# Kernel tuning notes

Measured on AMD Instinct MI355X. Metric: run time of the kernel, lower is better.

## Reference

```python
import jax, jax.numpy as jnp
import numpy as np

N, D = 8192, 128
TEMPERATURE = 0.07
EPS = 1e-8
NEG_FILL = -9e15


def setup_inputs() -> dict:
    key = jax.random.key(0)
    feats = jax.random.normal(key, (N, D), dtype=jnp.float32)
    # SimCLR-style positive-pair mask: row i's positive is row (i + N//2) % N.
    # Exactly one positive per row, as required by the original broadcast.
    label = jnp.roll(jnp.eye(N, dtype=jnp.int32), N // 2, axis=1)
    return {"feats": feats, "label": label}


def reference(feats, label):
    # F.cosine_similarity clamps each norm at eps before dividing.
    norms = jnp.linalg.norm(feats, axis=-1, keepdims=True)
    nf = feats / jnp.maximum(norms, EPS)            # [N, D] unit rows
    cos_sim = nf @ nf.T                             # [N, N] cosine similarities
    n = cos_sim.shape[0]
    self_mask = jnp.eye(n, dtype=bool)
    cos_sim = jnp.where(self_mask, NEG_FILL, cos_sim)
    cos_sim = cos_sim / TEMPERATURE
    pos_mask = (label == 1)
    # Exactly one positive per row -> masked sum == cos_sim[pos_mask] in row order.
    pos = jnp.sum(jnp.where(pos_mask, cos_sim, 0.0), axis=-1)  # [N]
    lse = jax.nn.logsumexp(cos_sim, axis=-1)                    # [N]
    return jnp.mean(-pos + lse)
```

## Files before the change

### kernel.cpp

```cpp
#include <hip/hip_runtime.h>


#define NN 8192
#define DD 128

typedef __bf16 bf16x8 __attribute__((ext_vector_type(8)));
typedef float f32x4 __attribute__((ext_vector_type(4)));
typedef unsigned int u32x4 __attribute__((ext_vector_type(4)));

constexpr float kM     = 1.0f / 0.07f;
constexpr float kScale = 1.4426950408889634f / 0.07f;
constexpr float kLn2   = 0.6931471805599453f;

__device__ inline unsigned short f2bf(float f) {
  unsigned int u = __float_as_uint(f);
  unsigned int r = (u + 0x7FFFu + ((u >> 16) & 1u)) >> 16;
  return (unsigned short)r;
}

__global__ __launch_bounds__(256) void k_normalize(const float* __restrict__ feats,
                                                   unsigned short* __restrict__ nfb) {
  int tid = threadIdx.x;
  int lane = tid & 63;
  int row = blockIdx.x * 4 + (tid >> 6);
  float2 f = *(const float2*)(feats + (size_t)row * DD + lane * 2);
  float ss = f.x * f.x + f.y * f.y;
  #pragma unroll
  for (int m = 1; m < 64; m <<= 1) ss += __shfl_xor(ss, m);
  float rn = 1.0f / fmaxf(sqrtf(ss), 1e-8f);
  unsigned int lo = f2bf(f.x * rn), hi = f2bf(f.y * rn);
  *(unsigned int*)(nfb + (size_t)row * DD + lane * 2) = lo | (hi << 16);
}

__global__ __launch_bounds__(256) void k_fused(const unsigned short* __restrict__ nfb,
                                               const int* __restrict__ label,
                                               float* __restrict__ lpart,
                                               int* __restrict__ pos_idx) {
  __shared__ __align__(16) unsigned short ldsB[64 * DD];
  int g = blockIdx.x;
  int tid = threadIdx.x;
  int r0 = (g >> 2) * 64;
  int c0 = (g & 3) * 2048;
  int lane = tid & 63, w = tid >> 6;
  int wm = w >> 1, wn = w & 1;
  int lg = lane >> 4;
  int ll = lane & 15;

  const u32x4* L = (const u32x4*)label;
  int sbase = g * 32768 + tid;

  bf16x8 afr[2][4];
  #pragma unroll
  for (int ms = 0; ms < 2; ms++) {
    const unsigned short* arow = nfb + (size_t)(r0 + wm * 32 + ms * 16 + ll) * DD + lg * 8;
    #pragma unroll
    for (int kc = 0; kc < 4; kc++)
      afr[ms][kc] = *(const bf16x8*)(arow + kc * 32);
  }

  float lacc[2][4] = {{0.f, 0.f, 0.f, 0.f}, {0.f, 0.f, 0.f, 0.f}};
  int slr = tid >> 4;
  int sch = tid & 15;

  for (int ct = 0; ct < 32; ct++) {
    int ctile = c0 + ct * 64;
    __syncthreads();
    #pragma unroll
    for (int p = 0; p < 4; p++) {
      int row = p * 16 + slr;
      u32x4 v = *(const u32x4*)(nfb + (size_t)(ctile + row) * DD + sch * 8);
      *(u32x4*)((char*)ldsB + row * 256 + ((sch * 16) ^ ((row & 7) << 4))) = v;
    }
    __syncthreads();

    u32x4 sv[4];
    #pragma unroll
    for (int j = 0; j < 4; j++)
      sv[j] = __builtin_nontemporal_load(&L[sbase + ct * 1024 + j * 256]);

    f32x4 acc[2][2] = {{{0.f,0.f,0.f,0.f},{0.f,0.f,0.f,0.f}},
                       {{0.f,0.f,0.f,0.f},{0.f,0.f,0.f,0.f}}};
    #pragma unroll
    for (int ns = 0; ns < 2; ns++) {
      int brow = wn * 32 + ns * 16 + ll;
      const char* bbase = (const char*)ldsB + brow * 256;
      int sw = (brow & 7) << 4;
      #pragma unroll
      for (int kc = 0; kc < 4; kc++) {
        bf16x8 bfr = *(const bf16x8*)(bbase + ((kc * 64 + lg * 16) ^ sw));
        acc[0][ns] = __builtin_amdgcn_mfma_f32_16x16x32_bf16(afr[0][kc], bfr, acc[0][ns], 0, 0, 0);
        acc[1][ns] = __builtin_amdgcn_mfma_f32_16x16x32_bf16(afr[1][kc], bfr, acc[1][ns], 0, 0, 0);
      }
    }

    bool mayDiag = (ctile < r0 + 64) && (r0 < ctile + 64);
    if (mayDiag) {
      #pragma unroll
      for (int ms = 0; ms < 2; ms++) {
        int growb = r0 + wm * 32 + ms * 16 + lg * 4;
        #pragma unroll
        for (int ns = 0; ns < 2; ns++) {
          int gcol = ctile + wn * 32 + ns * 16 + ll;
          #pragma unroll
          for (int r = 0; r < 4; r++) {
            float s = (growb + r == gcol) ? -3.0e38f : acc[ms][ns][r];
            lacc[ms][r] += __builtin_amdgcn_exp2f((s - 1.0f) * kScale);
          }
        }
      }
    } else {
      #pragma unroll
      for (int ms = 0; ms < 2; ms++)
        #pragma unroll
        for (int ns = 0; ns < 2; ns++)
          #pragma unroll
          for (int r = 0; r < 4; r++)
            lacc[ms][r] += __builtin_amdgcn_exp2f((acc[ms][ns][r] - 1.0f) * kScale);
    }

    unsigned any = 0;
    #pragma unroll
    for (int j = 0; j < 4; j++) any |= sv[j][0] | sv[j][1] | sv[j][2] | sv[j][3];
    if (any) {
      #pragma unroll
      for (int j = 0; j < 4; j++) {
        if (sv[j][0] | sv[j][1] | sv[j][2] | sv[j][3]) {
          int gi = (sbase + ct * 1024 + j * 256) * 4;
          int row = gi >> 13, col = gi & (NN - 1);
          if (sv[j][0] == 1u) pos_idx[row] = col;
          if (sv[j][1] == 1u) pos_idx[row] = col + 1;
          if (sv[j][2] == 1u) pos_idx[row] = col + 2;
          if (sv[j][3] == 1u) pos_idx[row] = col + 3;
        }
      }
    }
  }

  #pragma unroll
  for (int ms = 0; ms < 2; ms++)
    #pragma unroll
    for (int r = 0; r < 4; r++) {
      float v = lacc[ms][r];
      v += __shfl_xor(v, 1); v += __shfl_xor(v, 2);
      v += __shfl_xor(v, 4); v += __shfl_xor(v, 8);
      lacc[ms][r] = v;
    }
  if (ll == 0) {
    int slot = (g & 3) * 2 + wn;
    #pragma unroll
    for (int ms = 0; ms < 2; ms++)
      #pragma unroll
      for (int r = 0; r < 4; r++) {
        int grow = r0 + wm * 32 + ms * 16 + lg * 4 + r;
        lpart[(size_t)slot * NN + grow] = lacc[ms][r];
      }
  }
}

__global__ __launch_bounds__(256) void k_finalize(const unsigned short* __restrict__ nfb,
                                                  const float* __restrict__ lpart,
                                                  const int* __restrict__ pos_idx,
                                                  float* __restrict__ bpart) {
  int i = blockIdx.x * 256 + threadIdx.x;
  float l = 0.f;
  #pragma unroll
  for (int s = 0; s < 8; s++) l += lpart[(size_t)s * NN + i];
  float lse = kM + __builtin_amdgcn_logf(l) * kLn2;
  int p = pos_idx[i] & (NN - 1);
  const u32x4* ri = (const u32x4*)(nfb + (size_t)i * DD);
  const u32x4* rp = (const u32x4*)(nfb + (size_t)p * DD);
  float dot = 0.f;
  #pragma unroll
  for (int c = 0; c < 16; c++) {
    u32x4 a = ri[c], bb = rp[c];
    #pragma unroll
    for (int e = 0; e < 4; e++) {
      float al = __uint_as_float(a[e] << 16), ah = __uint_as_float(a[e] & 0xFFFF0000u);
      float bl = __uint_as_float(bb[e] << 16), bh = __uint_as_float(bb[e] & 0xFFFF0000u);
      dot += al * bl + ah * bh;
    }
  }
  float val = lse - dot * kM;
  #pragma unroll
  for (int m = 1; m < 64; m <<= 1) val += __shfl_xor(val, m);
  __shared__ float wsum[4];
  if ((threadIdx.x & 63) == 0) wsum[threadIdx.x >> 6] = val;
  __syncthreads();
  if (threadIdx.x == 0) bpart[blockIdx.x] = wsum[0] + wsum[1] + wsum[2] + wsum[3];
}

__global__ void k_reduce(const float* __restrict__ bpart, float* __restrict__ out) {
  int t = threadIdx.x;
  float v = (t < 32) ? bpart[t] : 0.f;
  #pragma unroll
  for (int m = 1; m < 64; m <<= 1) v += __shfl_xor(v, m);
  if (t == 0) out[0] = v * (1.0f / (float)NN);
}

extern "C" void kernel_launch(void* const* d_in, const int* in_sizes, int n_in,
                              void* d_out, int out_size, void* d_ws, size_t ws_size,
                              hipStream_t stream) {
  (void)in_sizes; (void)n_in; (void)out_size; (void)ws_size;
  const float* feats = (const float*)d_in[0];
  const int* label = (const int*)d_in[1];
  float* out = (float*)d_out;

  char* ws = (char*)d_ws;
  unsigned short* nfb = (unsigned short*)ws;
  float* lpart = (float*)(ws + 2 * 1024 * 1024);
  int* pos_idx = (int*)(ws + 2 * 1024 * 1024 + 262144);
  float* bpart = (float*)(ws + 2 * 1024 * 1024 + 262144 + 32768);

  k_normalize<<<NN / 4, 256, 0, stream>>>(feats, nfb);
  k_fused<<<512, 256, 0, stream>>>(nfb, label, lpart, pos_idx);
  k_finalize<<<NN / 256, 256, 0, stream>>>(nfb, lpart, pos_idx, bpart);
  k_reduce<<<1, 64, 0, stream>>>(bpart, out);
}
```

Before: 71.77 us.

## Drop LDS staging; each wave loads B fragments directly and owns a column quarter

Removes the shared-memory B tile and its two __syncthreads per iteration. Each wave now covers all 64 rows of the block over its own 512-column slice and loads B fragments straight from global/L2 into registers, issuing 8 MFMAs per B fragment. The label scan is remapped per wave, the lpart slots grow from 8 to 16, and the workspace offsets shift to match. The aim is to cut barrier stalls and LDS traffic, at the cost of four times more global B loads per block and higher register pressure under launch_bounds(256,2).

```diff
diff --git a/kernel.cpp b/kernel.cpp
--- a/kernel.cpp
+++ b/kernel.cpp
@@ -32,75 +32,77 @@
   *(unsigned int*)(nfb + (size_t)row * DD + lane * 2) = lo | (hi << 16);
 }
 
-__global__ __launch_bounds__(256) void k_fused(const unsigned short* __restrict__ nfb,
-                                               const int* __restrict__ label,
-                                               float* __restrict__ lpart,
-                                               int* __restrict__ pos_idx) {
-  __shared__ __align__(16) unsigned short ldsB[64 * DD];
+__global__ __launch_bounds__(256, 2) void k_fused(const unsigned short* __restrict__ nfb,
+                                                  const int* __restrict__ label,
+                                                  float* __restrict__ lpart,
+                                                  int* __restrict__ pos_idx) {
   int g = blockIdx.x;
   int tid = threadIdx.x;
-  int r0 = (g >> 2) * 64;
-  int c0 = (g & 3) * 2048;
-  int lane = tid & 63, w = tid >> 6;
-  int wm = w >> 1, wn = w & 1;
+  int w = tid >> 6;
+  int lane = tid & 63;
   int lg = lane >> 4;
   int ll = lane & 15;
 
+  int r0 = (g >> 2) * 64;
+  int cq = (g & 3) * 2048 + w * 512;
+  int wid = g * 4 + w;
+
   const u32x4* L = (const u32x4*)label;
-  int sbase = g * 32768 + tid;
-
-  bf16x8 afr[2][4];
-  #pragma unroll
-  for (int ms = 0; ms < 2; ms++) {
-    const unsigned short* arow = nfb + (size_t)(r0 + wm * 32 + ms * 16 + ll) * DD + lg * 8;
+  int sbase = wid * 8192 + lane;
+
+  bf16x8 afr[4][4];
+  #pragma unroll
+  for (int ms = 0; ms < 4; ms++) {
+    const unsigned short* arow = nfb + (size_t)(r0 + ms * 16 + ll) * DD + lg * 8;
     #pragma unroll
     for (int kc = 0; kc < 4; kc++)
       afr[ms][kc] = *(const bf16x8*)(arow + kc * 32);
   }
 
-  float lacc[2][4] = {{0.f, 0.f, 0.f, 0.f}, {0.f, 0.f, 0.f, 0.f}};
-  int slr = tid >> 4;
-  int sch = tid & 15;
-
-  for (int ct = 0; ct < 32; ct++) {
-    int ctile = c0 + ct * 64;
-    __syncthreads();
-    #pragma unroll
-    for (int p = 0; p < 4; p++) {
-      int row = p * 16 + slr;
-      u32x4 v = *(const u32x4*)(nfb + (size_t)(ctile + row) * DD + sch * 8);
-      *(u32x4*)((char*)ldsB + row * 256 + ((sch * 16) ^ ((row & 7) << 4))) = v;
-    }
-    __syncthreads();
-
-    u32x4 sv[4];
-    #pragma unroll
-    for (int j = 0; j < 4; j++)
-      sv[j] = __builtin_nontemporal_load(&L[sbase + ct * 1024 + j * 256]);
-
-    f32x4 acc[2][2] = {{{0.f,0.f,0.f,0.f},{0.f,0.f,0.f,0.f}},
-                       {{0.f,0.f,0.f,0.f},{0.f,0.f,0.f,0.f}}};
+  float lacc[4][4];
+  #pragma unroll
+  for (int ms = 0; ms < 4; ms++)
+    #pragma unroll
+    for (int r = 0; r < 4; r++) lacc[ms][r] = 0.f;
+
+  for (int it = 0; it < 16; ++it) {
+    int hcol = cq + it * 32;
+
+    bf16x8 bfr[2][4];
     #pragma unroll
     for (int ns = 0; ns < 2; ns++) {
-      int brow = wn * 32 + ns * 16 + ll;
-      const char* bbase = (const char*)ldsB + brow * 256;
-      int sw = (brow & 7) << 4;
-      #pragma unroll
-      for (int kc = 0; kc < 4; kc++) {
-        bf16x8 bfr = *(const bf16x8*)(bbase + ((kc * 64 + lg * 16) ^ sw));
-        acc[0][ns] = __builtin_amdgcn_mfma_f32_16x16x32_bf16(afr[0][kc], bfr, acc[0][ns], 0, 0, 0);
-        acc[1][ns] = __builtin_amdgcn_mfma_f32_16x16x32_bf16(afr[1][kc], bfr, acc[1][ns], 0, 0, 0);
-      }
-    }
-
-    bool mayDiag = (ctile < r0 + 64) && (r0 < ctile + 64);
+      const unsigned short* brow = nfb + (size_t)(hcol + ns * 16 + ll) * DD + lg * 8;
+      #pragma unroll
+      for (int kc = 0; kc < 4; kc++)
+        bfr[ns][kc] = *(const bf16x8*)(brow + kc * 32);
+    }
+
+    u32x4 sv[8];
+    #pragma unroll
+    for (int j = 0; j < 8; j++)
+      sv[j] = __builtin_nontemporal_load(&L[sbase + it * 512 + j * 64]);
+
+    f32x4 acc[4][2];
+    #pragma unroll
+    for (int ms = 0; ms < 4; ms++)
+      #pragma unroll
+      for (int ns = 0; ns < 2; ns++) acc[ms][ns] = (f32x4){0.f, 0.f, 0.f, 0.f};
+    #pragma unroll
+    for (int kc = 0; kc < 4; kc++)
+      #pragma unroll
+      for (int ns = 0; ns < 2; ns++)
+        #pragma unroll
+        for (int ms = 0; ms < 4; ms++)
+          acc[ms][ns] = __builtin_amdgcn_mfma_f32_16x16x32_bf16(afr[ms][kc], bfr[ns][kc], acc[ms][ns], 0, 0, 0);
+
+    bool mayDiag = (hcol < r0 + 64) && (hcol + 32 > r0);
     if (mayDiag) {
       #pragma unroll
-      for (int ms = 0; ms < 2; ms++) {
-        int growb = r0 + wm * 32 + ms * 16 + lg * 4;
+      for (int ms = 0; ms < 4; ms++) {
+        int growb = r0 + ms * 16 + lg * 4;
         #pragma unroll
         for (int ns = 0; ns < 2; ns++) {
-          int gcol = ctile + wn * 32 + ns * 16 + ll;
+          int gcol = hcol + ns * 16 + ll;
           #pragma unroll
           for (int r = 0; r < 4; r++) {
             float s = (growb + r == gcol) ? -3.0e38f : acc[ms][ns][r];
@@ -110,7 +112,7 @@
       }
     } else {
       #pragma unroll
-      for (int ms = 0; ms < 2; ms++)
+      for (int ms = 0; ms < 4; ms++)
         #pragma unroll
         for (int ns = 0; ns < 2; ns++)
           #pragma unroll
@@ -120,12 +122,12 @@
 
     unsigned any = 0;
     #pragma unroll
-    for (int j = 0; j < 4; j++) any |= sv[j][0] | sv[j][1] | sv[j][2] | sv[j][3];
+    for (int j = 0; j < 8; j++) any |= sv[j][0] | sv[j][1] | sv[j][2] | sv[j][3];
     if (any) {
       #pragma unroll
-      for (int j = 0; j < 4; j++) {
+      for (int j = 0; j < 8; j++) {
         if (sv[j][0] | sv[j][1] | sv[j][2] | sv[j][3]) {
-          int gi = (sbase + ct * 1024 + j * 256) * 4;
+          int gi = (sbase + it * 512 + j * 64) * 4;
           int row = gi >> 13, col = gi & (NN - 1);
           if (sv[j][0] == 1u) pos_idx[row] = col;
           if (sv[j][1] == 1u) pos_idx[row] = col + 1;
@@ -137,7 +139,7 @@
   }
 
   #pragma unroll
-  for (int ms = 0; ms < 2; ms++)
+  for (int ms = 0; ms < 4; ms++)
     #pragma unroll
     for (int r = 0; r < 4; r++) {
       float v = lacc[ms][r];
@@ -146,12 +148,12 @@
       lacc[ms][r] = v;
     }
   if (ll == 0) {
-    int slot = (g & 3) * 2 + wn;
-    #pragma unroll
-    for (int ms = 0; ms < 2; ms++)
+    int slot = (g & 3) * 4 + w;
+    #pragma unroll
+    for (int ms = 0; ms < 4; ms++)
       #pragma unroll
       for (int r = 0; r < 4; r++) {
-        int grow = r0 + wm * 32 + ms * 16 + lg * 4 + r;
+        int grow = r0 + ms * 16 + lg * 4 + r;
         lpart[(size_t)slot * NN + grow] = lacc[ms][r];
       }
   }
@@ -164,7 +166,7 @@
   int i = blockIdx.x * 256 + threadIdx.x;
   float l = 0.f;
   #pragma unroll
-  for (int s = 0; s < 8; s++) l += lpart[(size_t)s * NN + i];
+  for (int s = 0; s < 16; s++) l += lpart[(size_t)s * NN + i];
   float lse = kM + __builtin_amdgcn_logf(l) * kLn2;
   int p = pos_idx[i] & (NN - 1);
   const u32x4* ri = (const u32x4*)(nfb + (size_t)i * DD);
@@ -208,8 +210,8 @@
   char* ws = (char*)d_ws;
   unsigned short* nfb = (unsigned short*)ws;
   float* lpart = (float*)(ws + 2 * 1024 * 1024);
-  int* pos_idx = (int*)(ws + 2 * 1024 * 1024 + 262144);
-  float* bpart = (float*)(ws + 2 * 1024 * 1024 + 262144 + 32768);
+  int* pos_idx = (int*)(ws + 2 * 1024 * 1024 + 524288);
+  float* bpart = (float*)(ws + 2 * 1024 * 1024 + 524288 + 32768);
 
   k_normalize<<<NN / 4, 256, 0, stream>>>(feats, nfb);
   k_fused<<<512, 256, 0, stream>>>(nfb, label, lpart, pos_idx);
```

Measured after the change: 72.47 us. No clear change (+1.0%).
